# Kernel tuning notes

Hardware: AMD Instinct MI355X
Metric: run time of the kernel (lower is better)

## Reference

```python
import jax, jax.numpy as jnp
import numpy as np

EPS = 1e-8
THRESHOLD = 0.2

def setup_inputs() -> dict:
    key = jax.random.key(0)
    k1, k2 = jax.random.split(key)
    N, D, H = 8192, 256, 2
    x = jax.random.normal(k1, (N, D), dtype=jnp.float32)
    # per-head elementwise metric weight (MetricCalcLayer.weight, xavier-uniform init)
    bound = float(np.sqrt(6.0 / (1 + D)))
    w = jax.random.uniform(k2, (H, D), dtype=jnp.float32, minval=-bound, maxval=bound)
    K = 81  # int(N * 0.01), resolved top-k count per row
    return {"x": x, "w": w, "K": K}

def reference(x, w, K):
    # x: [N, D], w: [H, D]
    H = w.shape[0]
    N = x.shape[0]
    wx = x[None, :, :] * w[:, None, :]                       # [H, N, D]
    norms = jnp.linalg.norm(wx, axis=-1, keepdims=True)      # [H, N, 1]
    wn = wx / jnp.maximum(norms, EPS)                        # normalized per head
    # sum of per-head cosine similarity matrices, averaged over heads
    sim = jnp.einsum('hnd,hmd->nm', wn, wn) / H              # [N, N]
    # threshold (reverse=False): zero out entries below threshold
    sim = jnp.where(sim < THRESHOLD, jnp.zeros_like(sim), sim)
    # top-k per row -> scatter ones into a mask, multiply
    _, idx = jax.lax.top_k(sim, K)                           # [N, K]
    mask = jnp.zeros_like(sim).at[jnp.arange(N)[:, None], idx].set(1.0)
    return sim * mask
```

## Files before the change

kernel.cpp:

```cpp
#include <hip/hip_runtime.h>
#include <hip/hip_bf16.h>
#include <stdint.h>

#define NROWS 8192
#define DIM   256
#define KDIM  512
#define THRESH 0.2f
#define MARGIN 0.005f
#define FIX_CAP (1 << 20)
#define BLK_FIX_CAP 512
#define TOPK_CAP 4096

typedef __bf16 bf16x8 __attribute__((ext_vector_type(8)));
typedef float  f32x4  __attribute__((ext_vector_type(4)));

__device__ __forceinline__ void gload16(const void* g, void* l) {
  __builtin_amdgcn_global_load_lds(
      (const __attribute__((address_space(1))) uint32_t*)g,
      (__attribute__((address_space(3))) uint32_t*)l,
      16, 0, 0);
}

__global__ __launch_bounds__(256) void prep_k(const float* __restrict__ x,
                                              const float* __restrict__ w,
                                              ushort* __restrict__ z,
                                              int* __restrict__ cnt,
                                              int* __restrict__ fixn) {
  const int n = blockIdx.x;
  const int d = threadIdx.x;
  if (d == 0) cnt[n] = 0;
  if (n == 0 && d == 1) *fixn = 0;
  const float xv = x[(size_t)n * DIM + d];
  const float p0 = xv * w[d];
  const float p1 = xv * w[DIM + d];
  float s0 = p0 * p0, s1 = p1 * p1;
  #pragma unroll
  for (int off = 32; off > 0; off >>= 1) {
    s0 += __shfl_down(s0, off);
    s1 += __shfl_down(s1, off);
  }
  __shared__ float red0[4], red1[4];
  const int wv = d >> 6, ln = d & 63;
  if (ln == 0) { red0[wv] = s0; red1[wv] = s1; }
  __syncthreads();
  const float t0 = red0[0] + red0[1] + red0[2] + red0[3];
  const float t1 = red1[0] + red1[1] + red1[2] + red1[3];
  const float inv0 = 0.70710678118654752f / fmaxf(sqrtf(t0), 1e-8f);
  const float inv1 = 0.70710678118654752f / fmaxf(sqrtf(t1), 1e-8f);
  __hip_bfloat16 z0 = __float2bfloat16(p0 * inv0);
  __hip_bfloat16 z1 = __float2bfloat16(p1 * inv1);
  z[(size_t)n * KDIM + d]       = *(ushort*)&z0;
  z[(size_t)n * KDIM + DIM + d] = *(ushort*)&z1;
}

__global__ __launch_bounds__(256) void sim_gemm(const ushort* __restrict__ z,
                                               float* __restrict__ out,
                                               int* __restrict__ cnt,
                                               int* __restrict__ fixn,
                                               uint32_t* __restrict__ fixlist) {
  const int u = blockIdx.x;
  int bm = (int)((129.0 - sqrt(129.0 * 129.0 - 8.0 * (double)u)) * 0.5);
  if (bm > 63) bm = 63;
  while (bm * (129 - bm) / 2 > u) --bm;
  while ((bm + 1) * (129 - (bm + 1)) / 2 <= u) ++bm;
  const int bn = bm + (u - bm * (129 - bm) / 2);
  const bool offd = (bm != bn);

  __shared__ __align__(16) char smem[33280];
  ushort* ASb = (ushort*)smem;
  ushort* BSb = (ushort*)(smem + 16384);
  auto T2 = (float (*)[32][130])smem;
  __shared__ int cntA[128], cntB[128];
  __shared__ uint32_t fix_loc[BLK_FIX_CAP];
  __shared__ int fix_loc_n, fix_base;

  const int t = threadIdx.x;
  const int rowA = bm * 128, rowB = bn * 128;
  const int wv = t >> 6, lane = t & 63;
  const int wr = wv >> 1, wc = wv & 1;

  f32x4 acc[4][4];
  #pragma unroll
  for (int i = 0; i < 4; ++i)
    #pragma unroll
    for (int j = 0; j < 4; ++j) acc[i][j] = (f32x4)0.f;

  int aoff[4], boff[4];
  #pragma unroll
  for (int mi = 0; mi < 4; ++mi) {
    const int ar = wr * 64 + mi * 16 + (lane & 15);
    const int sw = (lane >> 4) ^ ((ar >> 1) & 3);
    aoff[mi] = ar * 32 + sw * 8;
  }
  #pragma unroll
  for (int ni = 0; ni < 4; ++ni) {
    const int br = wc * 64 + ni * 16 + (lane & 15);
    const int sw = (lane >> 4) ^ ((br >> 1) & 3);
    boff[ni] = br * 32 + sw * 8;
  }

  if (t < 128) { cntA[t] = 0; cntB[t] = 0; }
  if (t == 0) fix_loc_n = 0;

  const int i0 = t, r0 = i0 >> 2, s0_ = i0 & 3, cs0 = s0_ ^ ((r0 >> 1) & 3);
  const int i1 = t + 256, r1 = i1 >> 2, s1_ = i1 & 3, cs1 = s1_ ^ ((r1 >> 1) & 3);
  const ushort* zA0 = z + (size_t)(rowA + r0) * KDIM + cs0 * 8;
  const ushort* zB0 = z + (size_t)(rowB + r0) * KDIM + cs0 * 8;
  const ushort* zA1 = z + (size_t)(rowA + r1) * KDIM + cs1 * 8;
  const ushort* zB1 = z + (size_t)(rowB + r1) * KDIM + cs1 * 8;

  gload16(zA0,      ASb + (size_t)i0 * 8);
  gload16(zB0,      BSb + (size_t)i0 * 8);
  gload16(zA1,      ASb + (size_t)i1 * 8);
  gload16(zB1,      BSb + (size_t)i1 * 8);
  gload16(zA0 + 32, ASb + 4096 + (size_t)i0 * 8);
  gload16(zB0 + 32, BSb + 4096 + (size_t)i0 * 8);
  gload16(zA1 + 32, ASb + 4096 + (size_t)i1 * 8);
  gload16(zB1 + 32, BSb + 4096 + (size_t)i1 * 8);

  int cur = 0;
#define KSTEP(VMWAIT, STAGE_KB)                                                   \
  {                                                                               \
    asm volatile("s_waitcnt " VMWAIT ::: "memory");                               \
    __builtin_amdgcn_s_barrier();                                                 \
    __builtin_amdgcn_sched_barrier(0);                                            \
    const ushort* Ac = ASb + cur * 4096;                                          \
    const ushort* Bc = BSb + cur * 4096;                                          \
    bf16x8 af[4], bfv[4];                                                         \
    _Pragma("unroll")                                                             \
    for (int mi = 0; mi < 4; ++mi) af[mi] = *(const bf16x8*)(Ac + aoff[mi]);      \
    _Pragma("unroll")                                                             \
    for (int ni = 0; ni < 4; ++ni) bfv[ni] = *(const bf16x8*)(Bc + boff[ni]);     \
    asm volatile("s_waitcnt lgkmcnt(0)" ::: "memory");                            \
    __builtin_amdgcn_sched_barrier(0);                                            \
    __builtin_amdgcn_s_barrier();                                                 \
    __builtin_amdgcn_sched_barrier(0);                                            \
    if ((STAGE_KB) >= 0) {                                                        \
      const int kb = (STAGE_KB);                                                  \
      ushort* An = ASb + cur * 4096;                                              \
      ushort* Bn = BSb + cur * 4096;                                              \
      gload16(zA0 + kb, An + (size_t)i0 * 8);                                     \
      gload16(zB0 + kb, Bn + (size_t)i0 * 8);                                     \
      gload16(zA1 + kb, An + (size_t)i1 * 8);                                     \
      gload16(zB1 + kb, Bn + (size_t)i1 * 8);                                     \
    }                                                                             \
    _Pragma("unroll")                                                             \
    for (int mi = 0; mi < 4; ++mi)                                                \
      _Pragma("unroll")                                                           \
      for (int ni = 0; ni < 4; ++ni)                                              \
        acc[mi][ni] = __builtin_amdgcn_mfma_f32_16x16x32_bf16(af[mi], bfv[ni],    \
                                                              acc[mi][ni], 0, 0, 0); \
    cur ^= 1;                                                                     \
  }

  for (int kt = 0; kt < 14; ++kt) KSTEP("vmcnt(4)", (kt + 2) * 32);
  KSTEP("vmcnt(4)", -1);
  KSTEP("vmcnt(0)", -1);
#undef KSTEP

  #pragma unroll
  for (int mi = 0; mi < 4; ++mi) {
    #pragma unroll
    for (int ni = 0; ni < 4; ++ni) {
      const f32x4 v = acc[mi][ni];
      const int lc = wc * 64 + ni * 16 + (lane & 15);
      const int gc = rowB + lc;
      const int lrbase = wr * 64 + mi * 16 + (lane >> 4) * 4;
      #pragma unroll
      for (int r = 0; r < 4; ++r) {
        const float val = v[r];
        const int lr = lrbase + r;
        out[(size_t)(rowA + lr) * NROWS + gc] = (val < THRESH) ? 0.0f : val;
        if (val >= THRESH - MARGIN) {
          atomicAdd(&cntA[lr], 1);
          if (offd) atomicAdd(&cntB[lc], 1);
          if (val < THRESH + MARGIN) {
            const int p = atomicAdd(&fix_loc_n, 1);
            if (p < BLK_FIX_CAP) fix_loc[p] = (uint32_t)(rowA + lr) * NROWS + gc;
          }
        }
      }
    }
  }

  if (offd) {
    #pragma unroll
    for (int p = 0; p < 2; ++p) {
      __syncthreads();
      {
        const int c = p + 2 * wc;
        #pragma unroll
        for (int ni2 = 0; ni2 < 2; ++ni2) {
          const int ni = p * 2 + ni2;
          const int tc = ni2 * 16 + (lane & 15);
          #pragma unroll
          for (int mi = 0; mi < 4; ++mi) {
            const int lrb = wr * 64 + mi * 16 + (lane >> 4) * 4;
            #pragma unroll
            for (int r = 0; r < 4; ++r) T2[wc][tc][lrb + r] = acc[mi][ni][r];
          }
        }
      }
      __syncthreads();
      #pragma unroll
      for (int h = 0; h < 2; ++h) {
        const int c = p + 2 * h;
        #pragma unroll
        for (int it = 0; it < 8; ++it) {
          const int j = it * 4 + wv;
          const int i = (t & 63) * 2;
          float2 v2 = *(const float2*)&T2[h][j][i];
          v2.x = (v2.x < THRESH) ? 0.0f : v2.x;
          v2.y = (v2.y < THRESH) ? 0.0f : v2.y;
          *(float2*)&out[(size_t)(rowB + c * 32 + j) * NROWS + rowA + i] = v2;
        }
      }
    }
  }
  __syncthreads();

  if (t == 0) {
    int nf = fix_loc_n; if (nf > BLK_FIX_CAP) nf = BLK_FIX_CAP;
    fix_base = (nf > 0) ? atomicAdd(fixn, nf) : 0;
  }
  __syncthreads();
  {
    int nf = fix_loc_n; if (nf > BLK_FIX_CAP) nf = BLK_FIX_CAP;
    for (int i = t; i < nf; i += 256) {
      const int p = fix_base + i;
      if (p < FIX_CAP) fixlist[p] = fix_loc[i];
    }
    if (t < 128) {
      if (cntA[t] > 0) atomicAdd(&cnt[rowA + t], cntA[t]);
      if (offd && cntB[t] > 0) atomicAdd(&cnt[rowB + t], cntB[t]);
    }
  }
}

__global__ __launch_bounds__(256) void fix_k(const float* __restrict__ x,
                                             const float* __restrict__ w,
                                             float* __restrict__ out,
                                             const int* __restrict__ fixn,
                                             const uint32_t* __restrict__ fixlist) {
  const int wv = threadIdx.x >> 6, lane = threadIdx.x & 63;
  int total = *fixn;
  if (total > FIX_CAP) total = FIX_CAP;
  for (int e = blockIdx.x * 4 + wv; e < total; e += gridDim.x * 4) {
    const uint32_t f = fixlist[e];
    const int r = (int)(f / NROWS), c = (int)(f % NROWS);
    double dot0 = 0, dot1 = 0, nr0 = 0, nr1 = 0, nc0 = 0, nc1 = 0;
    #pragma unroll
    for (int i2 = 0; i2 < DIM / 64; ++i2) {
      const int i = i2 * 64 + lane;
      const double w0 = (double)w[i],              w1 = (double)w[DIM + i];
      const double xr = (double)x[(size_t)r * DIM + i];
      const double xc = (double)x[(size_t)c * DIM + i];
      const double pr0 = xr * w0, pc0 = xc * w0;
      const double pr1 = xr * w1, pc1 = xc * w1;
      dot0 += pr0 * pc0; nr0 += pr0 * pr0; nc0 += pc0 * pc0;
      dot1 += pr1 * pc1; nr1 += pr1 * pr1; nc1 += pc1 * pc1;
    }
    #pragma unroll
    for (int off = 32; off > 0; off >>= 1) {
      dot0 += __shfl_down(dot0, off); nr0 += __shfl_down(nr0, off); nc0 += __shfl_down(nc0, off);
      dot1 += __shfl_down(dot1, off); nr1 += __shfl_down(nr1, off); nc1 += __shfl_down(nc1, off);
    }
    if (lane == 0) {
      const double s0 = dot0 / (fmax(sqrt(nr0), 1e-8) * fmax(sqrt(nc0), 1e-8));
      const double s1 = dot1 / (fmax(sqrt(nr1), 1e-8) * fmax(sqrt(nc1), 1e-8));
      const double sim = 0.5 * (s0 + s1);
      const float res = (sim < (double)THRESH) ? 0.0f : (float)sim;
      out[(size_t)r * NROWS + c] = res;
      out[(size_t)c * NROWS + r] = res;
    }
  }
}

__global__ __launch_bounds__(256) void topk_fix(float* __restrict__ out,
                                                const int* __restrict__ cnt,
                                                const int* __restrict__ Kp) {
  const int row = blockIdx.x;
  const int K = Kp[0];
  if (cnt[row] <= K) return;

  __shared__ float vals[TOPK_CAP];
  __shared__ int   idxs[TOPK_CAP];
  __shared__ int   num;
  if (threadIdx.x == 0) num = 0;
  __syncthreads();
  for (int j = threadIdx.x; j < NROWS; j += 256) {
    const float v = out[(size_t)row * NROWS + j];
    if (v != 0.0f) {
      const int p = atomicAdd(&num, 1);
      if (p < TOPK_CAP) { vals[p] = v; idxs[p] = j; }
    }
  }
  __syncthreads();
  const int c = (num < TOPK_CAP) ? num : TOPK_CAP;
  for (int p = threadIdx.x; p < c; p += 256) {
    const float v = vals[p];
    const int  id = idxs[p];
    int rank = 0;
    for (int q = 0; q < c; ++q) {
      const float u = vals[q];
      rank += (u > v) || (u == v && idxs[q] < id);
    }
    if (rank >= K) out[(size_t)row * NROWS + id] = 0.0f;
  }
}

extern "C" void kernel_launch(void* const* d_in, const int* in_sizes, int n_in,
                              void* d_out, int out_size, void* d_ws, size_t ws_size,
                              hipStream_t stream) {
  const float* x  = (const float*)d_in[0];
  const float* w  = (const float*)d_in[1];
  const int*   Kp = (const int*)d_in[2];
  float* out = (float*)d_out;

  char* ws = (char*)d_ws;
  ushort*   z       = (ushort*)ws;
  int*      cnt     = (int*)(ws + (size_t)NROWS * KDIM * 2);
  int*      fixn    = (int*)(ws + (size_t)NROWS * KDIM * 2 + NROWS * 4);
  uint32_t* fixlist = (uint32_t*)(ws + (size_t)NROWS * KDIM * 2 + NROWS * 4 + 256);

  prep_k<<<NROWS, 256, 0, stream>>>(x, w, z, cnt, fixn);
  sim_gemm<<<2080, 256, 0, stream>>>(z, out, cnt, fixn, fixlist);
  fix_k<<<2048, 256, 0, stream>>>(x, w, out, fixn, fixlist);
  topk_fix<<<NROWS, 256, 0, stream>>>(out, cnt, Kp);
}
```

Baseline: 131.5 us.

## Fuse near-threshold fp64 fixup into GEMM epilogue and use nontemporal stores

Removes the separate fix_k kernel and its global fixlist/atomic counter. Each GEMM block now recomputes its own near-threshold entries in double precision right after writing its tile, so one launch and the global list traffic go away. Output stores become nontemporal so the large 256MB result does not pollute cache. The risk is a longer tail in blocks with many fix entries, and fp64 work now sits inside the GEMM blocks.

```diff
diff --git a/kernel.cpp b/kernel.cpp
--- a/kernel.cpp
+++ b/kernel.cpp
@@ -7,12 +7,12 @@
 #define KDIM  512
 #define THRESH 0.2f
 #define MARGIN 0.005f
-#define FIX_CAP (1 << 20)
 #define BLK_FIX_CAP 512
 #define TOPK_CAP 4096
 
 typedef __bf16 bf16x8 __attribute__((ext_vector_type(8)));
 typedef float  f32x4  __attribute__((ext_vector_type(4)));
+typedef float  f32x2  __attribute__((ext_vector_type(2)));
 
 __device__ __forceinline__ void gload16(const void* g, void* l) {
   __builtin_amdgcn_global_load_lds(
@@ -24,12 +24,10 @@
 __global__ __launch_bounds__(256) void prep_k(const float* __restrict__ x,
                                               const float* __restrict__ w,
                                               ushort* __restrict__ z,
-                                              int* __restrict__ cnt,
-                                              int* __restrict__ fixn) {
+                                              int* __restrict__ cnt) {
   const int n = blockIdx.x;
   const int d = threadIdx.x;
   if (d == 0) cnt[n] = 0;
-  if (n == 0 && d == 1) *fixn = 0;
   const float xv = x[(size_t)n * DIM + d];
   const float p0 = xv * w[d];
   const float p1 = xv * w[DIM + d];
@@ -54,10 +52,10 @@
 }
 
 __global__ __launch_bounds__(256) void sim_gemm(const ushort* __restrict__ z,
+                                               const float* __restrict__ x,
+                                               const float* __restrict__ w,
                                                float* __restrict__ out,
-                                               int* __restrict__ cnt,
-                                               int* __restrict__ fixn,
-                                               uint32_t* __restrict__ fixlist) {
+                                               int* __restrict__ cnt) {
   const int u = blockIdx.x;
   int bm = (int)((129.0 - sqrt(129.0 * 129.0 - 8.0 * (double)u)) * 0.5);
   if (bm > 63) bm = 63;
@@ -72,7 +70,7 @@
   auto T2 = (float (*)[32][130])smem;
   __shared__ int cntA[128], cntB[128];
   __shared__ uint32_t fix_loc[BLK_FIX_CAP];
-  __shared__ int fix_loc_n, fix_base;
+  __shared__ int fix_loc_n;
 
   const int t = threadIdx.x;
   const int rowA = bm * 128, rowB = bn * 128;
@@ -170,7 +168,8 @@
       for (int r = 0; r < 4; ++r) {
         const float val = v[r];
         const int lr = lrbase + r;
-        out[(size_t)(rowA + lr) * NROWS + gc] = (val < THRESH) ? 0.0f : val;
+        __builtin_nontemporal_store((val < THRESH) ? 0.0f : val,
+                                    &out[(size_t)(rowA + lr) * NROWS + gc]);
         if (val >= THRESH - MARGIN) {
           atomicAdd(&cntA[lr], 1);
           if (offd) atomicAdd(&cntB[lc], 1);
@@ -209,70 +208,53 @@
         for (int it = 0; it < 8; ++it) {
           const int j = it * 4 + wv;
           const int i = (t & 63) * 2;
-          float2 v2 = *(const float2*)&T2[h][j][i];
+          f32x2 v2 = *(const f32x2*)&T2[h][j][i];
           v2.x = (v2.x < THRESH) ? 0.0f : v2.x;
           v2.y = (v2.y < THRESH) ? 0.0f : v2.y;
-          *(float2*)&out[(size_t)(rowB + c * 32 + j) * NROWS + rowA + i] = v2;
+          __builtin_nontemporal_store(v2,
+              (f32x2*)&out[(size_t)(rowB + c * 32 + j) * NROWS + rowA + i]);
         }
       }
     }
   }
   __syncthreads();
 
-  if (t == 0) {
-    int nf = fix_loc_n; if (nf > BLK_FIX_CAP) nf = BLK_FIX_CAP;
-    fix_base = (nf > 0) ? atomicAdd(fixn, nf) : 0;
-  }
-  __syncthreads();
   {
-    int nf = fix_loc_n; if (nf > BLK_FIX_CAP) nf = BLK_FIX_CAP;
-    for (int i = t; i < nf; i += 256) {
-      const int p = fix_base + i;
-      if (p < FIX_CAP) fixlist[p] = fix_loc[i];
-    }
-    if (t < 128) {
-      if (cntA[t] > 0) atomicAdd(&cnt[rowA + t], cntA[t]);
-      if (offd && cntB[t] > 0) atomicAdd(&cnt[rowB + t], cntB[t]);
-    }
-  }
-}
-
-__global__ __launch_bounds__(256) void fix_k(const float* __restrict__ x,
-                                             const float* __restrict__ w,
-                                             float* __restrict__ out,
-                                             const int* __restrict__ fixn,
-                                             const uint32_t* __restrict__ fixlist) {
-  const int wv = threadIdx.x >> 6, lane = threadIdx.x & 63;
-  int total = *fixn;
-  if (total > FIX_CAP) total = FIX_CAP;
-  for (int e = blockIdx.x * 4 + wv; e < total; e += gridDim.x * 4) {
-    const uint32_t f = fixlist[e];
-    const int r = (int)(f / NROWS), c = (int)(f % NROWS);
-    double dot0 = 0, dot1 = 0, nr0 = 0, nr1 = 0, nc0 = 0, nc1 = 0;
-    #pragma unroll
-    for (int i2 = 0; i2 < DIM / 64; ++i2) {
-      const int i = i2 * 64 + lane;
-      const double w0 = (double)w[i],              w1 = (double)w[DIM + i];
-      const double xr = (double)x[(size_t)r * DIM + i];
-      const double xc = (double)x[(size_t)c * DIM + i];
-      const double pr0 = xr * w0, pc0 = xc * w0;
-      const double pr1 = xr * w1, pc1 = xc * w1;
-      dot0 += pr0 * pc0; nr0 += pr0 * pr0; nc0 += pc0 * pc0;
-      dot1 += pr1 * pc1; nr1 += pr1 * pr1; nc1 += pc1 * pc1;
-    }
-    #pragma unroll
-    for (int off = 32; off > 0; off >>= 1) {
-      dot0 += __shfl_down(dot0, off); nr0 += __shfl_down(nr0, off); nc0 += __shfl_down(nc0, off);
-      dot1 += __shfl_down(dot1, off); nr1 += __shfl_down(nr1, off); nc1 += __shfl_down(nc1, off);
-    }
-    if (lane == 0) {
-      const double s0 = dot0 / (fmax(sqrt(nr0), 1e-8) * fmax(sqrt(nc0), 1e-8));
-      const double s1 = dot1 / (fmax(sqrt(nr1), 1e-8) * fmax(sqrt(nc1), 1e-8));
-      const double sim = 0.5 * (s0 + s1);
-      const float res = (sim < (double)THRESH) ? 0.0f : (float)sim;
-      out[(size_t)r * NROWS + c] = res;
-      out[(size_t)c * NROWS + r] = res;
-    }
+    const int nf = (fix_loc_n < BLK_FIX_CAP) ? fix_loc_n : BLK_FIX_CAP;
+    for (int e = wv; e < nf; e += 4) {
+      const uint32_t f = fix_loc[e];
+      const int r = (int)(f / NROWS), c = (int)(f % NROWS);
+      double dot0 = 0, dot1 = 0, nr0 = 0, nr1 = 0, nc0 = 0, nc1 = 0;
+      #pragma unroll
+      for (int i2 = 0; i2 < DIM / 64; ++i2) {
+        const int i = i2 * 64 + lane;
+        const double w0 = (double)w[i],              w1 = (double)w[DIM + i];
+        const double xr = (double)x[(size_t)r * DIM + i];
+        const double xc = (double)x[(size_t)c * DIM + i];
+        const double pr0 = xr * w0, pc0 = xc * w0;
+        const double pr1 = xr * w1, pc1 = xc * w1;
+        dot0 += pr0 * pc0; nr0 += pr0 * pr0; nc0 += pc0 * pc0;
+        dot1 += pr1 * pc1; nr1 += pr1 * pr1; nc1 += pc1 * pc1;
+      }
+      #pragma unroll
+      for (int off = 32; off > 0; off >>= 1) {
+        dot0 += __shfl_down(dot0, off); nr0 += __shfl_down(nr0, off); nc0 += __shfl_down(nc0, off);
+        dot1 += __shfl_down(dot1, off); nr1 += __shfl_down(nr1, off); nc1 += __shfl_down(nc1, off);
+      }
+      if (lane == 0) {
+        const double s0 = dot0 / (fmax(sqrt(nr0), 1e-8) * fmax(sqrt(nc0), 1e-8));
+        const double s1 = dot1 / (fmax(sqrt(nr1), 1e-8) * fmax(sqrt(nc1), 1e-8));
+        const double sim = 0.5 * (s0 + s1);
+        const float res = (sim < (double)THRESH) ? 0.0f : (float)sim;
+        out[(size_t)r * NROWS + c] = res;
+        out[(size_t)c * NROWS + r] = res;
+      }
+    }
+  }
+
+  if (t < 128) {
+    if (cntA[t] > 0) atomicAdd(&cnt[rowA + t], cntA[t]);
+    if (offd && cntB[t] > 0) atomicAdd(&cnt[rowB + t], cntB[t]);
   }
 }
 
@@ -318,13 +300,10 @@
   float* out = (float*)d_out;
 
   char* ws = (char*)d_ws;
-  ushort*   z       = (ushort*)ws;
-  int*      cnt     = (int*)(ws + (size_t)NROWS * KDIM * 2);
-  int*      fixn    = (int*)(ws + (size_t)NROWS * KDIM * 2 + NROWS * 4);
-  uint32_t* fixlist = (uint32_t*)(ws + (size_t)NROWS * KDIM * 2 + NROWS * 4 + 256);
-
-  prep_k<<<NROWS, 256, 0, stream>>>(x, w, z, cnt, fixn);
-  sim_gemm<<<2080, 256, 0, stream>>>(z, out, cnt, fixn, fixlist);
-  fix_k<<<2048, 256, 0, stream>>>(x, w, out, fixn, fixlist);
+  ushort* z   = (ushort*)ws;
+  int*    cnt = (int*)(ws + (size_t)NROWS * KDIM * 2);
+
+  prep_k<<<NROWS, 256, 0, stream>>>(x, w, z, cnt);
+  sim_gemm<<<2080, 256, 0, stream>>>(z, x, w, out, cnt);
   topk_fix<<<NROWS, 256, 0, stream>>>(out, cnt, Kp);
 }
```

Result: slower. 136.5 us (+3.8%).
